# Kernel tuning notes

Hardware: AMD Instinct MI355X
Metric: run time of the kernel (lower is better)

Reference implementation:

```python
import jax, jax.numpy as jnp
import numpy as np

BN_INV = 1.0 / np.float32(np.sqrt(1.0 + 1e-5))  # eval BN with running_mean=0, running_var=1


def _conv(x, w, stride):
    return jax.lax.conv_general_dilated(
        x, w, (stride, stride), [(1, 1), (1, 1)],
        dimension_numbers=('NCHW', 'OIHW', 'NCHW'))


def _se(x, w1, b1, w2, b2):
    # squeeze-excite: global avg pool -> fc -> relu -> fc -> sigmoid -> scale
    y = x.mean(axis=(2, 3))                       # (B, C)
    y = jax.nn.relu(y @ w1.T + b1)
    y = jax.nn.sigmoid(y @ w2.T + b2)
    return x * y[:, :, None, None]


def _squash(s):
    n2 = jnp.sum(s * s, axis=-1, keepdims=True)
    n = jnp.sqrt(n2)
    return s * (n2 / (1.0 + n2)) / (n + 1e-8)


def _block(x, cw, g, b, s1w, s1b, s2w, s2b, stride):
    h = _conv(x, cw, stride)
    h = h * (g * BN_INV)[None, :, None, None] + b[None, :, None, None]
    h = jax.nn.relu(h)
    return _se(h, s1w, s1b, s2w, s2b)


def setup_inputs() -> dict:
    key = jax.random.key(0)
    ks = jax.random.split(key, 32)
    rn = lambda i, shape, s=1.0: s * jax.random.normal(ks[i], shape, dtype=jnp.float32)
    d = {}
    d['x'] = rn(0, (64, 1, 128, 128))
    # feature extractor
    d['conv1_w'] = rn(1, (16, 1, 3, 3), 0.3)
    d['bn1_g'] = 1.0 + rn(2, (16,), 0.1)
    d['bn1_b'] = rn(3, (16,), 0.1)
    d['se1_w1'] = rn(4, (1, 16), 0.2); d['se1_b1'] = rn(5, (1,), 0.1)
    d['se1_w2'] = rn(6, (16, 1), 0.2); d['se1_b2'] = rn(7, (16,), 0.1)
    d['conv2_w'] = rn(8, (32, 16, 3, 3), 0.1)
    d['bn2_g'] = 1.0 + rn(9, (32,), 0.1)
    d['bn2_b'] = rn(10, (32,), 0.1)
    d['se2_w1'] = rn(11, (2, 32), 0.2); d['se2_b1'] = rn(12, (2,), 0.1)
    d['se2_w2'] = rn(13, (32, 2), 0.2); d['se2_b2'] = rn(14, (32,), 0.1)
    d['conv3_w'] = rn(15, (64, 32, 3, 3), 0.07)
    d['bn3_g'] = 1.0 + rn(16, (64,), 0.1)
    d['bn3_b'] = rn(17, (64,), 0.1)
    d['se3_w1'] = rn(18, (4, 64), 0.15); d['se3_b1'] = rn(19, (4,), 0.1)
    d['se3_w2'] = rn(20, (64, 4), 0.15); d['se3_b2'] = rn(21, (64,), 0.1)
    # primary capsules conv: 64 -> 8 caps * 8 dim = 64 channels, stride 2
    d['pc_w'] = rn(22, (64, 64, 3, 3), 0.05)
    d['pc_b'] = rn(23, (64,), 0.05)
    # digit capsule transform: (1, 2048, 3, 16, 8)
    d['W_digit'] = 0.01 * jax.random.normal(ks[24], (1, 2048, 3, 16, 8), dtype=jnp.float32)
    return d


def reference(x, conv1_w, bn1_g, bn1_b, se1_w1, se1_b1, se1_w2, se1_b2,
              conv2_w, bn2_g, bn2_b, se2_w1, se2_b1, se2_w2, se2_b2,
              conv3_w, bn3_g, bn3_b, se3_w1, se3_b1, se3_w2, se3_b2,
              pc_w, pc_b, W_digit):
    h = _block(x, conv1_w, bn1_g, bn1_b, se1_w1, se1_b1, se1_w2, se1_b2, 1)
    h = _block(h, conv2_w, bn2_g, bn2_b, se2_w1, se2_b1, se2_w2, se2_b2, 2)
    h = _block(h, conv3_w, bn3_g, bn3_b, se3_w1, se3_b1, se3_w2, se3_b2, 2)
    # primary capsules: conv -> (B, 8 caps, 8 dim, 16*16) -> (B, 2048, 8)
    u = _conv(h, pc_w, 2) + pc_b[None, :, None, None]     # (B, 64, 16, 16)
    B = u.shape[0]
    u = u.reshape(B, 8, 8, -1).transpose(0, 1, 3, 2).reshape(B, -1, 8)
    u = _squash(u)                                        # (B, 2048, 8)
    # u_hat[b,i,c,d] = sum_e W[0,i,c,d,e] * u[b,i,e]  (avoids torch's W.repeat)
    u_hat = jnp.einsum('icde,bie->bicd', W_digit[0], u)   # (B, 2048, 3, 16)
    b_ij = jnp.zeros((B, u_hat.shape[1], u_hat.shape[2], 1), u_hat.dtype)
    v_j = None
    for _ in range(3):  # fixed routing iterations
        c_ij = jax.nn.softmax(b_ij, axis=2)
        s_j = jnp.sum(c_ij * u_hat, axis=1, keepdims=True)  # (B,1,3,16)
        v_j = _squash(s_j)
        b_ij = b_ij + jnp.sum(u_hat * v_j, axis=-1, keepdims=True)
    v = v_j[:, 0]                                          # (B, 3, 16)
    return jnp.sqrt(jnp.sum(v * v, axis=-1))               # (B, 3) class lengths
```

## Files before the change

kernel.cpp:

```cpp
#include <hip/hip_runtime.h>
#include <math.h>

#define BN_INV_F 0.9999950000374997f

__device__ __forceinline__ void gload_lds4(const float* g, float* l) {
    __builtin_amdgcn_global_load_lds(
        (const __attribute__((address_space(1))) void*)g,
        (__attribute__((address_space(3))) void*)l, 4, 0, 0);
}

__global__ __launch_bounds__(256) void wtrans_all_k(
    const float* __restrict__ w1, const float* __restrict__ w2,
    const float* __restrict__ w3, const float* __restrict__ wp,
    float* __restrict__ w1t, float* __restrict__ w2t,
    float* __restrict__ w3t, float* __restrict__ wpt)
{
    int i = blockIdx.x * 256 + threadIdx.x;
    if (i < 144) {
        int co = i % 16, k = i / 16;
        w1t[i] = w1[co * 9 + k];
    } else if (i < 4752) {
        int t = i - 144;
        int co = t % 32, rk = t / 32, cin = rk / 9, k = rk % 9;
        w2t[t] = w2[(co * 16 + cin) * 9 + k];
    } else if (i < 23184) {
        int t = i - 4752;
        int co = t % 64, rk = t / 64, cin = rk / 9, k = rk % 9;
        w3t[t] = w3[(co * 32 + cin) * 9 + k];
    } else if (i < 60048) {
        int t = i - 23184;
        int co = t % 64, rk = t / 64, cin = rk / 9, k = rk % 9;
        wpt[t] = wp[(co * 64 + cin) * 9 + k];
    }
}

template <int CIN, int CINB, int COUT, int COB, int HIN, int HOUT, int STRIDE,
          int TW, int ROWS_T, int PPT, int CB, int NTHREADS,
          bool BN_RELU, bool SE_SUM, int HSE_IN, int KSPLIT>
__global__ __launch_bounds__(NTHREADS) void convt_k(
    const float* __restrict__ in, const float* __restrict__ wt,
    const float* __restrict__ gamma,
    const float* __restrict__ beta,
    float* __restrict__ out, size_t pstride,
    float* __restrict__ se_sum,
    const float* __restrict__ se_sums_in,
    const float* __restrict__ se_w1, const float* __restrict__ se_b1,
    const float* __restrict__ se_w2, const float* __restrict__ se_b2,
    float inv_spatial)
{
    constexpr int WIN = HIN, WOUT = HOUT;
    constexpr int TH = ROWS_T * PPT;
    constexpr int IH_T = (TH - 1) * STRIDE + 3;
    constexpr int NW = NTHREADS / 64;
    constexpr int NCHUNK = CINB / CB;
    constexpr int SEGS = (WIN >= 64) ? (WIN / 64) : 1;
    constexpr int PAIRS = (IH_T + 1) / 2;
    constexpr int NG = COUT / COB;
    static_assert(NTHREADS == TW * ROWS_T, "geometry");
    static_assert(TW == WOUT, "tile must span full output width");
    static_assert(CINB % CB == 0, "chunking");
    static_assert(WIN % 64 == 0 || WIN == 32, "stage width");

    const int b = blockIdx.z;
    const int gy = blockIdx.y;
    const int ty = blockIdx.x;
    const int tid = threadIdx.x;
    const int wo = tid % TW;
    const int rg = tid / TW;
    const int g = gy % NG;
    const int kk = gy / NG;
    const int cin0 = kk * CINB;

    __shared__ float in_t[2][CB * IH_T * WIN];
    __shared__ float scl[CIN];
    __shared__ float gl[COB], bl[COB];
    __shared__ float red[NW][COB];
    __shared__ float hid[HSE_IN > 0 ? HSE_IN : 1];

    const float* inb = in + (size_t)b * CIN * HIN * WIN;
    const int gr0 = ty * TH * STRIDE - 1;
    const int wos = wo * STRIDE;
    const int wvid = tid >> 6, lane = tid & 63;

    auto stage = [&](int c, int buf) {
        const int cb0 = cin0 + c * CB;
        float* bb = &in_t[buf][0];
        if (WIN >= 64) {
            for (int r = wvid; r < CB * IH_T; r += NW) {
                int ci = r / IH_T, lr = r - ci * IH_T;
                int gr = gr0 + lr;
                float* ldst = bb + (ci * IH_T + lr) * WIN;
                if (gr >= 0 && gr < HIN) {
                    const float* gsrc = inb + (size_t)(cb0 + ci) * HIN * WIN + (size_t)gr * WIN;
#pragma unroll
                    for (int s = 0; s < SEGS; ++s)
                        gload_lds4(gsrc + s * 64 + lane, ldst + s * 64);
                } else {
#pragma unroll
                    for (int s = 0; s < SEGS; ++s) ldst[s * 64 + lane] = 0.0f;
                }
            }
        } else {
            for (int pz = wvid; pz < CB * PAIRS; pz += NW) {
                int ci = pz / PAIRS, q = pz - ci * PAIRS;
                int lr0 = q * 2;
                int nr = (lr0 + 1 < IH_T) ? 2 : 1;
                int grr = gr0 + lr0;
                float* ldst = bb + (ci * IH_T + lr0) * WIN;
                if (nr == 2 && grr >= 0 && grr + 1 < HIN) {
                    const float* gsrc = inb + (size_t)(cb0 + ci) * HIN * WIN + (size_t)grr * WIN + lane;
                    gload_lds4(gsrc, ldst);
                } else {
                    for (int e = lane; e < nr * WIN; e += 64) {
                        int rr = e / WIN, cc = e - rr * WIN;
                        int gr = grr + rr;
                        ldst[e] = (gr >= 0 && gr < HIN)
                            ? inb[(size_t)(cb0 + ci) * HIN * WIN + (size_t)gr * WIN + cc] : 0.0f;
                    }
                }
            }
        }
    };

    stage(0, 0);

    if (HSE_IN > 0) {
        if (tid < HSE_IN) {
            float a = se_b1[tid];
            for (int c = 0; c < CIN; ++c)
                a = fmaf(se_sums_in[b * CIN + c] * inv_spatial, se_w1[tid * CIN + c], a);
            hid[tid] = fmaxf(a, 0.0f);
        }
        __syncthreads();
        if (tid < CIN) {
            float a = se_b2[tid];
            for (int h = 0; h < HSE_IN; ++h)
                a = fmaf(hid[h], se_w2[tid * HSE_IN + h], a);
            scl[tid] = 1.0f / (1.0f + expf(-a));
        }
    } else {
        for (int t = tid; t < CIN; t += NTHREADS) scl[t] = 1.0f;
    }
    if (tid < COB) {
        int co = g * COB + tid;
        if (BN_RELU) {
            gl[tid] = gamma[co] * BN_INV_F;
            bl[tid] = beta[co];
        } else {
            gl[tid] = (kk == 0) ? gamma[co] : 0.0f;
        }
    }

    float acc[PPT][COB];
#pragma unroll
    for (int p = 0; p < PPT; ++p)
#pragma unroll
        for (int co = 0; co < COB; ++co) acc[p][co] = 0.0f;

    int cur = 0;
    for (int c = 0; c < NCHUNK; ++c) {
        asm volatile("s_waitcnt vmcnt(0)" ::: "memory");
        __syncthreads();
        if (c + 1 < NCHUNK) stage(c + 1, cur ^ 1);

        const float* bb = &in_t[cur][0];
        for (int ci = 0; ci < CB; ++ci) {
            const int cw = cin0 + c * CB + ci;
            const float sc = scl[cw];
            const float* wtap = wt + (size_t)cw * 9 * COUT + g * COB;
#pragma unroll
            for (int kh = 0; kh < 3; ++kh) {
#pragma unroll
                for (int kw = 0; kw < 3; ++kw) {
                    const float* wrow = wtap + (kh * 3 + kw) * COUT;
#pragma unroll
                    for (int p = 0; p < PPT; ++p) {
                        const float* row = bb + (ci * IH_T + (rg + p * ROWS_T) * STRIDE + kh) * WIN;
                        int wi = wos + kw - 1;
                        float v;
                        if (kw == 0) {
                            v = row[wi < 0 ? 0 : wi];
                            if (wi < 0) v = 0.0f;
                        } else if (STRIDE == 1 && kw == 2) {
                            v = row[wi >= WIN ? WIN - 1 : wi];
                            if (wi >= WIN) v = 0.0f;
                        } else {
                            v = row[wi];
                        }
                        v *= sc;
#pragma unroll
                        for (int co = 0; co < COB; ++co)
                            acc[p][co] = fmaf(wrow[co], v, acc[p][co]);
                    }
                }
            }
        }
        cur ^= 1;
    }

    float tsum[COB];
#pragma unroll
    for (int co = 0; co < COB; ++co) tsum[co] = 0.0f;
    float* ob = out + (size_t)kk * pstride
              + ((size_t)b * COUT + (size_t)g * COB) * HOUT * WOUT;
#pragma unroll
    for (int p = 0; p < PPT; ++p) {
        const int ho = ty * TH + rg + p * ROWS_T;
#pragma unroll
        for (int co = 0; co < COB; ++co) {
            float v;
            if (BN_RELU)
                v = fmaxf(fmaf(acc[p][co], gl[co], bl[co]), 0.0f);
            else
                v = acc[p][co] + gl[co];
            ob[(size_t)co * HOUT * WOUT + ho * WOUT + wo] = v;
            tsum[co] += v;
        }
    }

    if (SE_SUM) {
#pragma unroll
        for (int co = 0; co < COB; ++co) {
            float v = tsum[co];
            for (int off = 32; off; off >>= 1) v += __shfl_down(v, off, 64);
            if (lane == 0) red[wvid][co] = v;
        }
        __syncthreads();
        if (tid < COB) {
            float v = 0.0f;
#pragma unroll
            for (int k = 0; k < NW; ++k) v += red[k][tid];
            atomicAdd(&se_sum[b * COUT + g * COB + tid], v);
        }
    }
}

__global__ __launch_bounds__(256) void cb_k(const float* __restrict__ pA,
                                            const float* __restrict__ pB,
                                            const float* __restrict__ gamma,
                                            const float* __restrict__ beta,
                                            float* __restrict__ h3,
                                            float* __restrict__ s3)
{
    const int bc = blockIdx.x;
    const int c = bc & 63;
    const int tid = threadIdx.x;
    __shared__ float red[4];
    const size_t base = (size_t)bc * 1024;
    float4 a = ((const float4*)(pA + base))[tid];
    float4 d = ((const float4*)(pB + base))[tid];
    const float g = gamma[c] * BN_INV_F, be = beta[c];
    float4 v;
    v.x = fmaxf(fmaf(a.x + d.x, g, be), 0.0f);
    v.y = fmaxf(fmaf(a.y + d.y, g, be), 0.0f);
    v.z = fmaxf(fmaf(a.z + d.z, g, be), 0.0f);
    v.w = fmaxf(fmaf(a.w + d.w, g, be), 0.0f);
    ((float4*)(h3 + base))[tid] = v;
    float s = (v.x + v.y) + (v.z + v.w);
    for (int off = 32; off; off >>= 1) s += __shfl_down(s, off, 64);
    const int lane = tid & 63, wv = tid >> 6;
    if (lane == 0) red[wv] = s;
    __syncthreads();
    if (tid == 0) s3[bc] = (red[0] + red[1]) + (red[2] + red[3]);
}

__global__ __launch_bounds__(256) void squash4_k(const float* __restrict__ up,
                                                 size_t pstride,
                                                 float* __restrict__ u)
{
    const int idx = blockIdx.x * 256 + threadIdx.x;
    const int b = idx >> 11, i = idx & 2047;
    const int chi = i >> 8, spx = i & 255;
    const size_t off = ((size_t)(b * 64 + chi * 8)) * 256 + spx;
    float s[8];
    float n2 = 0.0f;
#pragma unroll
    for (int j = 0; j < 8; j++) {
        const size_t o = off + (size_t)j * 256;
        s[j] = (up[o] + up[o + pstride]) + (up[o + 2 * pstride] + up[o + 3 * pstride]);
        n2 = fmaf(s[j], s[j], n2);
    }
    const float n = sqrtf(n2);
    const float f = (n2 / (1.0f + n2)) / (n + 1e-8f);
    float* q = u + (size_t)idx * 8;
#pragma unroll
    for (int j = 0; j < 8; j++) q[j] = s[j] * f;
}

__global__ __launch_bounds__(256) void uhat_k(const float* __restrict__ u,
                                              const float* __restrict__ W,
                                              float* __restrict__ u_hat)
{
    const int idx = blockIdx.x * 256 + threadIdx.x;
    const int cd = idx % 48;
    const int bi = idx / 48;
    const int i = bi & 2047;
    const float* uu = u + (size_t)bi * 8;
    const float* wp = W + (size_t)i * 384 + cd * 8;
    float a = 0.0f;
#pragma unroll
    for (int e = 0; e < 8; e++) a = fmaf(wp[e], uu[e], a);
    u_hat[idx] = a;
}

template <int IT>
__global__ __launch_bounds__(256) void sweep_k(const float* __restrict__ u_hat,
                                               const float* __restrict__ s_hist,
                                               float* __restrict__ s_out)
{
    const int b = blockIdx.y;
    const int i = blockIdx.x * 256 + threadIdx.x;
    const int tid = threadIdx.x;
    __shared__ float vsh[IT > 0 ? IT : 1][48];
    __shared__ float fac[IT > 0 ? IT : 1][3];
    __shared__ float red[4][48];

    const float4* qp = (const float4*)(u_hat + ((size_t)b * 2048 + i) * 48);
    float uhv[48];
#pragma unroll
    for (int q = 0; q < 12; ++q) {
        float4 t = qp[q];
        uhv[q * 4 + 0] = t.x; uhv[q * 4 + 1] = t.y;
        uhv[q * 4 + 2] = t.z; uhv[q * 4 + 3] = t.w;
    }

    if (IT > 0) {
        if (tid < IT * 48) {
            int t = tid / 48, c = tid % 48;
            vsh[t][c] = s_hist[((size_t)t * 64 + b) * 48 + c];
        }
        __syncthreads();
        if (tid < IT * 3) {
            int t = tid / 3, j = tid % 3;
            float n2 = 0.0f;
            for (int d = 0; d < 16; ++d) { float s = vsh[t][j * 16 + d]; n2 = fmaf(s, s, n2); }
            float n = sqrtf(n2);
            fac[t][j] = (n2 / (1.0f + n2)) / (n + 1e-8f);
        }
        __syncthreads();
        if (tid < IT * 48) {
            int t = tid / 48, c = tid % 48;
            vsh[t][c] *= fac[t][c / 16];
        }
        __syncthreads();
    }

    float c0, c1, c2;
    if (IT == 0) {
        c0 = c1 = c2 = (1.0f / 3.0f);
    } else {
        float b0 = 0.0f, b1 = 0.0f, b2 = 0.0f;
#pragma unroll
        for (int t = 0; t < IT; ++t)
#pragma unroll
            for (int d = 0; d < 16; ++d) {
                b0 = fmaf(uhv[d],      vsh[t][d],      b0);
                b1 = fmaf(uhv[16 + d], vsh[t][16 + d], b1);
                b2 = fmaf(uhv[32 + d], vsh[t][32 + d], b2);
            }
        float m = fmaxf(b0, fmaxf(b1, b2));
        float e0 = expf(b0 - m), e1 = expf(b1 - m), e2 = expf(b2 - m);
        float inv = 1.0f / (e0 + e1 + e2);
        c0 = e0 * inv; c1 = e1 * inv; c2 = e2 * inv;
    }

    float sp[48];
#pragma unroll
    for (int d = 0; d < 16; ++d) {
        sp[d]      = c0 * uhv[d];
        sp[16 + d] = c1 * uhv[16 + d];
        sp[32 + d] = c2 * uhv[32 + d];
    }
    const int lane = tid & 63, wv = tid >> 6;
#pragma unroll
    for (int j = 0; j < 48; ++j) {
        float x = sp[j];
        for (int off = 32; off; off >>= 1) x += __shfl_down(x, off, 64);
        if (lane == 0) red[wv][j] = x;
    }
    __syncthreads();
    if (tid < 48) {
        float x = red[0][tid] + red[1][tid] + red[2][tid] + red[3][tid];
        atomicAdd(&s_out[(size_t)b * 48 + tid], x);
    }
}

__global__ __launch_bounds__(64) void route_out_k(const float* __restrict__ s2,
                                                  float* __restrict__ out)
{
    const int b = blockIdx.x;
    __shared__ float s[48];
    if (threadIdx.x < 48) s[threadIdx.x] = s2[(size_t)b * 48 + threadIdx.x];
    __syncthreads();
    if (threadIdx.x < 3) {
        int j = threadIdx.x;
        float n2 = 0.0f;
        for (int d = 0; d < 16; ++d) { float v = s[j * 16 + d]; n2 = fmaf(v, v, n2); }
        float n = sqrtf(n2);
        float fc = (n2 / (1.0f + n2)) / (n + 1e-8f);
        out[b * 3 + j] = fc * n;
    }
}

extern "C" void kernel_launch(void* const* d_in, const int* in_sizes, int n_in,
                              void* d_out, int out_size, void* d_ws, size_t ws_size,
                              hipStream_t stream)
{
    const float* x       = (const float*)d_in[0];
    const float* conv1_w = (const float*)d_in[1];
    const float* bn1_g   = (const float*)d_in[2];
    const float* bn1_b   = (const float*)d_in[3];
    const float* se1_w1  = (const float*)d_in[4];
    const float* se1_b1  = (const float*)d_in[5];
    const float* se1_w2  = (const float*)d_in[6];
    const float* se1_b2  = (const float*)d_in[7];
    const float* conv2_w = (const float*)d_in[8];
    const float* bn2_g   = (const float*)d_in[9];
    const float* bn2_b   = (const float*)d_in[10];
    const float* se2_w1  = (const float*)d_in[11];
    const float* se2_b1  = (const float*)d_in[12];
    const float* se2_w2  = (const float*)d_in[13];
    const float* se2_b2  = (const float*)d_in[14];
    const float* conv3_w = (const float*)d_in[15];
    const float* bn3_g   = (const float*)d_in[16];
    const float* bn3_b   = (const float*)d_in[17];
    const float* se3_w1  = (const float*)d_in[18];
    const float* se3_b1  = (const float*)d_in[19];
    const float* se3_w2  = (const float*)d_in[20];
    const float* se3_b2  = (const float*)d_in[21];
    const float* pc_w    = (const float*)d_in[22];
    const float* pc_b    = (const float*)d_in[23];
    const float* W_digit = (const float*)d_in[24];

    float* ws = (float*)d_ws;
    float* h1     = ws;
    float* h2     = ws + 16777216;
    float* h3     = ws;
    float* cp0    = ws + 4194304;
    float* cp1    = ws + 8388608;
    float* uparts = ws + 4194304;
    float* u      = ws + 8388608;
    float* u_hat  = ws + 9437184;
    float* sums   = ws + 25165824;
    float* s1 = sums, *s2 = sums + 1024, *s3 = sums + 3072;
    float* s_buf  = sums + 7168;
    float* zeros64 = sums + 16384;
    float* w1t    = ws + 25182272;
    float* w2t    = w1t + 144;
    float* w3t    = w2t + 4608;
    float* wpt    = w3t + 18432;

    hipMemsetAsync(sums, 0, 16448 * sizeof(float), stream);
    wtrans_all_k<<<235, 256, 0, stream>>>(conv1_w, conv2_w, conv3_w, pc_w,
                                          w1t, w2t, w3t, wpt);

    convt_k<1, 1, 16, 16, 128, 128, 1, 128, 2, 2, 1, 256, true, true, 0, 1>
        <<<dim3(32, 1, 64), 256, 0, stream>>>(
            x, w1t, bn1_g, bn1_b, h1, 0, s1,
            nullptr, nullptr, nullptr, nullptr, nullptr, 0.0f);

    convt_k<16, 16, 32, 32, 128, 64, 2, 64, 4, 1, 4, 256, true, true, 1, 1>
        <<<dim3(16, 1, 64), 256, 0, stream>>>(
            h1, w2t, bn2_g, bn2_b, h2, 0, s2,
            s1, se1_w1, se1_b1, se1_w2, se1_b2, 1.0f / 16384.0f);

    convt_k<32, 16, 64, 32, 64, 32, 2, 32, 8, 1, 4, 256, false, false, 2, 2>
        <<<dim3(4, 4, 64), 256, 0, stream>>>(
            h2, w3t, zeros64, nullptr, cp0, (size_t)4194304, nullptr,
            s2, se2_w1, se2_b1, se2_w2, se2_b2, 1.0f / 4096.0f);

    cb_k<<<4096, 256, 0, stream>>>(cp0, cp1, bn3_g, bn3_b, h3, s3);

    convt_k<64, 16, 64, 16, 32, 16, 2, 16, 16, 1, 4, 256, false, false, 4, 4>
        <<<dim3(1, 16, 64), 256, 0, stream>>>(
            h3, wpt, pc_b, nullptr, uparts, (size_t)1048576, nullptr,
            s3, se3_w1, se3_b1, se3_w2, se3_b2, 1.0f / 1024.0f);

    squash4_k<<<512, 256, 0, stream>>>(uparts, (size_t)1048576, u);
    uhat_k<<<24576, 256, 0, stream>>>(u, W_digit, u_hat);

    sweep_k<0><<<dim3(8, 64), 256, 0, stream>>>(u_hat, s_buf, s_buf + 0 * 64 * 48);
    sweep_k<1><<<dim3(8, 64), 256, 0, stream>>>(u_hat, s_buf, s_buf + 1 * 64 * 48);
    sweep_k<2><<<dim3(8, 64), 256, 0, stream>>>(u_hat, s_buf, s_buf + 2 * 64 * 48);
    route_out_k<<<64, 64, 0, stream>>>(s_buf + 2 * 64 * 48, (float*)d_out);
}
```

Before: 228.7 us.

## Fuse squash with u_hat transform and retile conv2 launch

Merges the primary-capsule squash kernel and the u_hat einsum kernel into one kernel. The squashed capsule vectors stay in shared memory, so the intermediate u buffer is never written to or read back from global memory, and one launch is removed. The conv2 launch also changes its tile parameters to 128 threads per block with twice as many blocks, and the per-chunk channel loop in the conv kernel is fully unrolled. The fused kernel launches only 512 blocks for the u_hat work instead of 24576, which lowers parallelism in that phase.

```diff
diff --git a/kernel.cpp b/kernel.cpp
--- a/kernel.cpp
+++ b/kernel.cpp
@@ -164,6 +164,7 @@
         if (c + 1 < NCHUNK) stage(c + 1, cur ^ 1);
 
         const float* bb = &in_t[cur][0];
+#pragma unroll
         for (int ci = 0; ci < CB; ++ci) {
             const int cw = cin0 + c * CB + ci;
             const float sc = scl[cw];
@@ -264,43 +265,46 @@
     if (tid == 0) s3[bc] = (red[0] + red[1]) + (red[2] + red[3]);
 }
 
-__global__ __launch_bounds__(256) void squash4_k(const float* __restrict__ up,
-                                                 size_t pstride,
-                                                 float* __restrict__ u)
-{
-    const int idx = blockIdx.x * 256 + threadIdx.x;
-    const int b = idx >> 11, i = idx & 2047;
-    const int chi = i >> 8, spx = i & 255;
-    const size_t off = ((size_t)(b * 64 + chi * 8)) * 256 + spx;
-    float s[8];
-    float n2 = 0.0f;
-#pragma unroll
-    for (int j = 0; j < 8; j++) {
-        const size_t o = off + (size_t)j * 256;
-        s[j] = (up[o] + up[o + pstride]) + (up[o + 2 * pstride] + up[o + 3 * pstride]);
-        n2 = fmaf(s[j], s[j], n2);
-    }
-    const float n = sqrtf(n2);
-    const float f = (n2 / (1.0f + n2)) / (n + 1e-8f);
-    float* q = u + (size_t)idx * 8;
-#pragma unroll
-    for (int j = 0; j < 8; j++) q[j] = s[j] * f;
-}
-
-__global__ __launch_bounds__(256) void uhat_k(const float* __restrict__ u,
-                                              const float* __restrict__ W,
-                                              float* __restrict__ u_hat)
-{
-    const int idx = blockIdx.x * 256 + threadIdx.x;
-    const int cd = idx % 48;
-    const int bi = idx / 48;
-    const int i = bi & 2047;
-    const float* uu = u + (size_t)bi * 8;
-    const float* wp = W + (size_t)i * 384 + cd * 8;
-    float a = 0.0f;
-#pragma unroll
-    for (int e = 0; e < 8; e++) a = fmaf(wp[e], uu[e], a);
-    u_hat[idx] = a;
+__global__ __launch_bounds__(256) void squash_uhat_k(
+    const float* __restrict__ up, size_t pstride,
+    const float* __restrict__ W, float* __restrict__ u_hat)
+{
+    const int base = blockIdx.x * 256;
+    const int tid = threadIdx.x;
+    __shared__ float ush[256][8];
+
+    {
+        const int cap = base + tid;
+        const int b = cap >> 11, i = cap & 2047;
+        const int chi = i >> 8, spx = i & 255;
+        const size_t off = ((size_t)(b * 64 + chi * 8)) * 256 + spx;
+        float s[8];
+        float n2 = 0.0f;
+#pragma unroll
+        for (int j = 0; j < 8; j++) {
+            const size_t o = off + (size_t)j * 256;
+            s[j] = (up[o] + up[o + pstride]) + (up[o + 2 * pstride] + up[o + 3 * pstride]);
+            n2 = fmaf(s[j], s[j], n2);
+        }
+        const float n = sqrtf(n2);
+        const float f = (n2 / (1.0f + n2)) / (n + 1e-8f);
+#pragma unroll
+        for (int j = 0; j < 8; j++) ush[tid][j] = s[j] * f;
+    }
+    __syncthreads();
+
+    float* ob = u_hat + (size_t)base * 48;
+#pragma unroll 4
+    for (int k = 0; k < 48; ++k) {
+        int o = tid + k * 256;
+        int c = o / 48, cd = o % 48;
+        int gi = (base + c) & 2047;
+        const float* wp = W + (size_t)gi * 384 + cd * 8;
+        float a = 0.0f;
+#pragma unroll
+        for (int e = 0; e < 8; e++) a = fmaf(wp[e], ush[c][e], a);
+        ob[o] = a;
+    }
 }
 
 template <int IT>
@@ -439,7 +443,6 @@
     float* cp0    = ws + 4194304;
     float* cp1    = ws + 8388608;
     float* uparts = ws + 4194304;
-    float* u      = ws + 8388608;
     float* u_hat  = ws + 9437184;
     float* sums   = ws + 25165824;
     float* s1 = sums, *s2 = sums + 1024, *s3 = sums + 3072;
@@ -459,8 +462,8 @@
             x, w1t, bn1_g, bn1_b, h1, 0, s1,
             nullptr, nullptr, nullptr, nullptr, nullptr, 0.0f);
 
-    convt_k<16, 16, 32, 32, 128, 64, 2, 64, 4, 1, 4, 256, true, true, 1, 1>
-        <<<dim3(16, 1, 64), 256, 0, stream>>>(
+    convt_k<16, 16, 32, 32, 128, 64, 2, 64, 2, 1, 4, 128, true, true, 1, 1>
+        <<<dim3(32, 1, 64), 128, 0, stream>>>(
             h1, w2t, bn2_g, bn2_b, h2, 0, s2,
             s1, se1_w1, se1_b1, se1_w2, se1_b2, 1.0f / 16384.0f);
 
@@ -476,8 +479,7 @@
             h3, wpt, pc_b, nullptr, uparts, (size_t)1048576, nullptr,
             s3, se3_w1, se3_b1, se3_w2, se3_b2, 1.0f / 1024.0f);
 
-    squash4_k<<<512, 256, 0, stream>>>(uparts, (size_t)1048576, u);
-    uhat_k<<<24576, 256, 0, stream>>>(u, W_digit, u_hat);
+    squash_uhat_k<<<512, 256, 0, stream>>>(uparts, (size_t)1048576, W_digit, u_hat);
 
     sweep_k<0><<<dim3(8, 64), 256, 0, stream>>>(u_hat, s_buf, s_buf + 0 * 64 * 48);
     sweep_k<1><<<dim3(8, 64), 256, 0, stream>>>(u_hat, s_buf, s_buf + 1 * 64 * 48);
```

Result: slower. 252.5 us (+10.4%).
